# Kernel optimization log

Measured on AMD Instinct MI355X. Metric: run time of the kernel, lower is better.

## Reference

```python
import jax, jax.numpy as jnp
import numpy as np

N = 50000
LN_EPS = 1e-5
NEG_SLOPE = 0.2


def layer_norm(x, w, b):
    mu = jnp.mean(x, axis=-1, keepdims=True)
    var = jnp.mean((x - mu) ** 2, axis=-1, keepdims=True)
    return (x - mu) * jax.lax.rsqrt(var + LN_EPS) * w + b


def gat_conv(x, src, dst, W, a_src, a_dst, bias, concat):
    # W: [in, H*D]; a_src/a_dst: [H, D]
    H, D = a_src.shape
    h = (x @ W).reshape(-1, H, D)                      # [N, H, D]
    s = jnp.einsum('nhd,hd->nh', h, a_src)             # alpha contribution of source
    t = jnp.einsum('nhd,hd->nh', h, a_dst)             # alpha contribution of target
    e = jax.nn.leaky_relu(s[src] + t[dst], NEG_SLOPE)  # [E, H] edge logits
    m = jax.ops.segment_max(e, dst, num_segments=N)    # segment softmax over incoming edges
    p = jnp.exp(e - m[dst])
    z = jax.ops.segment_sum(p, dst, num_segments=N)
    alpha = p / (z[dst] + 1e-16)                       # [E, H]
    out = jax.ops.segment_sum(alpha[:, :, None] * h[src], dst, num_segments=N)  # [N, H, D]
    out = out.reshape(N, H * D) if concat else out.mean(axis=1)
    return out + bias


def setup_inputs() -> dict:
    key = jax.random.key(0)
    ks = jax.random.split(key, 16)
    IN, HID, OUT, H1, H2 = 256, 32, 40, 6, 3
    E = 800000
    g = lambda k, shp, fan: jax.random.normal(k, shp, jnp.float32) * (1.0 / np.sqrt(fan))
    inp = {
        'x': jax.random.normal(ks[0], (N, IN), jnp.float32),
        'edge_index': jax.random.randint(ks[1], (2, E), 0, N, jnp.int32),
        'W1': g(ks[2], (IN, H1 * HID), IN), 'a1s': g(ks[3], (H1, HID), HID), 'a1d': g(ks[4], (H1, HID), HID),
        'b1': jnp.zeros((H1 * HID,), jnp.float32),
        'ln1w': jnp.ones((H1 * HID,), jnp.float32), 'ln1b': jnp.zeros((H1 * HID,), jnp.float32),
        'W2': g(ks[5], (H1 * HID, H2 * HID), H1 * HID), 'a2s': g(ks[6], (H2, HID), HID), 'a2d': g(ks[7], (H2, HID), HID),
        'b2': jnp.zeros((H2 * HID,), jnp.float32),
        'ln2w': jnp.ones((H2 * HID,), jnp.float32), 'ln2b': jnp.zeros((H2 * HID,), jnp.float32),
        'W3': g(ks[8], (H2 * HID, 1 * OUT), H2 * HID), 'a3s': g(ks[9], (1, OUT), OUT), 'a3d': g(ks[10], (1, OUT), OUT),
        'b3': jnp.zeros((OUT,), jnp.float32),
        'ln3w': jnp.ones((OUT,), jnp.float32), 'ln3b': jnp.zeros((OUT,), jnp.float32),
    }
    return inp


def reference(x, edge_index, W1, a1s, a1d, b1, ln1w, ln1b,
              W2, a2s, a2d, b2, ln2w, ln2b,
              W3, a3s, a3d, b3, ln3w, ln3b):
    # add self-loops (PyG GATConv default); eval mode -> dropouts are identity
    loop = jnp.arange(N, dtype=edge_index.dtype)
    src = jnp.concatenate([edge_index[0], loop])
    dst = jnp.concatenate([edge_index[1], loop])

    h = gat_conv(x, src, dst, W1, a1s, a1d, b1, concat=True)
    h = jax.nn.elu(layer_norm(h, ln1w, ln1b))
    h = gat_conv(h, src, dst, W2, a2s, a2d, b2, concat=True)
    h = jax.nn.elu(layer_norm(h, ln2w, ln2b))
    h = gat_conv(h, src, dst, W3, a3s, a3d, b3, concat=False)
    h = layer_norm(h, ln3w, ln3b)
    return jax.nn.log_softmax(h, axis=1)
```

## Files before the change

kernel.cpp:

```cpp
#include <hip/hip_runtime.h>
#include <hip/hip_bf16.h>
#include <cstdint>

#define NNODES 50000
#define NEDGES 800000
#define ETOT   (NEDGES + NNODES)
#define LN_EPS 1e-5f
#define NEG_SLOPE 0.2f
#define ELLW   64

typedef __attribute__((ext_vector_type(8))) short s16x8;
typedef __attribute__((ext_vector_type(4))) float f32x4;

__device__ __forceinline__ float bf2f(unsigned short u) {
    return __uint_as_float(((unsigned int)u) << 16);
}
__device__ __forceinline__ unsigned short f2bf(float f) {
    unsigned int u = __float_as_uint(f);
    u += 0x7FFFu + ((u >> 16) & 1u);
    return (unsigned short)(u >> 16);
}
__device__ __forceinline__ float plo32(unsigned u) { return __uint_as_float(u << 16); }
__device__ __forceinline__ float phi32(unsigned u) { return __uint_as_float(u & 0xffff0000u); }


#define W1SZ (192 * 256)
#define W2SZ (96 * 192)
#define W3SZ (48 * 96)

__global__ __launch_bounds__(256) void prep_kernel(const float* __restrict__ W1, const float* __restrict__ W2,
                                                   const float* __restrict__ W3, unsigned short* __restrict__ wt1,
                                                   unsigned short* __restrict__ wt2, unsigned short* __restrict__ wt3,
                                                   int* __restrict__ counts, int* __restrict__ ell) {
    int i = blockIdx.x * 256 + threadIdx.x;
    if (i < NNODES) {
        counts[i] = 1;
        ell[i * ELLW] = i;
    }
    if (i < W1SZ) {
        int c = i >> 8, k = i & 255;
        int n = c >> 4, r = c & 15;
        wt1[((n * 32 + (k >> 3)) * 16 + r) * 8 + (k & 7)] = f2bf(W1[k * 192 + c]);
    } else if (i < W1SZ + W2SZ) {
        int j = i - W1SZ;
        int c = j / 192, k = j - c * 192;
        int n = c >> 4, r = c & 15;
        wt2[((n * 24 + (k >> 3)) * 16 + r) * 8 + (k & 7)] = f2bf(W2[k * 96 + c]);
    } else if (i < W1SZ + W2SZ + W3SZ) {
        int j = i - (W1SZ + W2SZ);
        int c = j / 96, k = j - c * 96;
        int n = c >> 4, r = c & 15;
        wt3[((n * 12 + (k >> 3)) * 16 + r) * 8 + (k & 7)] = (c < 40) ? f2bf(W3[k * 40 + c]) : (unsigned short)0;
    }
}


__global__ __launch_bounds__(256) void fill_ell_kernel(const int* __restrict__ eidx, int* counts,
                                                       int* __restrict__ ell, int e) {
    int i = blockIdx.x * blockDim.x + threadIdx.x;
    if (i >= e) return;
    int sv = eidx[i];
    int d  = eidx[e + i];
    int slot = atomicAdd(&counts[d], 1);
    if (slot < ELLW) ell[d * ELLW + slot] = sv;
}


template<int K, int F, int CS, int FP, bool ABF>
__global__ __launch_bounds__(256) void mfma_gemm_kernel(const void* __restrict__ Xv,
                                                        const unsigned short* __restrict__ Wt,
                                                        unsigned short* __restrict__ C, int nrows) {
    constexpr int NT = FP / 16;
    int gw = (blockIdx.x * blockDim.x + threadIdx.x) >> 6;
    int lane = threadIdx.x & 63;
    int mbase = gw * 16;
    if (mbase >= nrows) return;
    const int r = lane & 15;
    const int q = lane >> 4;

    f32x4 acc[NT];
#pragma unroll
    for (int n = 0; n < NT; ++n) acc[n] = (f32x4){0.f, 0.f, 0.f, 0.f};

    int arow = mbase + r;
    if (arow >= nrows) arow = nrows - 1;
    const unsigned short* xb = (const unsigned short*)Xv + (size_t)arow * K;
    const float* xf = (const float*)Xv + (size_t)arow * K;

    for (int k0 = 0; k0 < K; k0 += 32) {
        const int kk = k0 + q * 8;
        const unsigned kc = (unsigned)(kk >> 3);
        s16x8 a;
        if constexpr (ABF) {
            a = *reinterpret_cast<const s16x8*>(xb + kk);
        } else {
            float4 lo = *reinterpret_cast<const float4*>(xf + kk);
            float4 hi = *reinterpret_cast<const float4*>(xf + kk + 4);
            a[0] = (short)f2bf(lo.x); a[1] = (short)f2bf(lo.y);
            a[2] = (short)f2bf(lo.z); a[3] = (short)f2bf(lo.w);
            a[4] = (short)f2bf(hi.x); a[5] = (short)f2bf(hi.y);
            a[6] = (short)f2bf(hi.z); a[7] = (short)f2bf(hi.w);
        }
#pragma unroll
        for (int n = 0; n < NT; ++n) {
            s16x8 b = *reinterpret_cast<const s16x8*>(Wt + (((unsigned)n * (K / 8) + kc) * 16 + (unsigned)r) * 8);
            acc[n] = __builtin_amdgcn_mfma_f32_16x16x32_bf16(a, b, acc[n], 0, 0, 0);
        }
    }
#pragma unroll
    for (int n = 0; n < NT; ++n) {
        int col = n * 16 + r;
        if (col < F) {
#pragma unroll
            for (int i = 0; i < 4; ++i) {
                int row = mbase + q * 4 + i;
                if (row < nrows) C[(size_t)row * CS + col] = f2bf(acc[n][i]);
            }
        }
    }
}


template<int H, int D, int FS, int SPAD>
__global__ __launch_bounds__(256) void st_kernel(const unsigned short* __restrict__ feat,
                                                 const float* __restrict__ as, const float* __restrict__ ad,
                                                 float* __restrict__ s, float* __restrict__ tt, int n) {
    int i = blockIdx.x * blockDim.x + threadIdx.x;
    if (i >= n * H) return;
    int h = i % H;
    int node = i / H;
    const ushort4* row = reinterpret_cast<const ushort4*>(feat + (size_t)node * FS + h * D);
    float ss = 0.f, td = 0.f;
#pragma unroll
    for (int d4 = 0; d4 < D / 4; ++d4) {
        ushort4 u = row[d4];
        float v0 = bf2f(u.x), v1 = bf2f(u.y), v2 = bf2f(u.z), v3 = bf2f(u.w);
        int d = d4 * 4;
        ss += v0 * as[h * D + d] + v1 * as[h * D + d + 1] + v2 * as[h * D + d + 2] + v3 * as[h * D + d + 3];
        td += v0 * ad[h * D + d] + v1 * ad[h * D + d + 1] + v2 * ad[h * D + d + 2] + v3 * ad[h * D + d + 3];
    }
    s[node * SPAD + h] = ss;
    tt[i] = td;
}


template<int H, int D, int FS, int CPL, int SPAD, int MODE, typename OutT>
__global__ __launch_bounds__(256) void agg7_kernel(const unsigned short* __restrict__ feat,
                                                   const float* __restrict__ sb, const float* __restrict__ tb,
                                                   const int* __restrict__ counts, const int* __restrict__ ell,
                                                   const float* __restrict__ bias, const float* __restrict__ lnw,
                                                   const float* __restrict__ lnb, OutT* __restrict__ out, int n) {
    constexpr int F = H * D;
    constexpr int NL = F / CPL;
    int wid = (blockIdx.x * blockDim.x + threadIdx.x) >> 6;
    int lane = threadIdx.x & 63;
    if (wid >= n) return;
    const int node = wid;
    const int base = node * ELLW;
    int cnt = counts[node];
    if (cnt > ELLW) cnt = ELLW;
    const bool act = lane < NL;
    const unsigned ch0 = (unsigned)(lane < NL ? lane : 0) * CPL;
    const int h = (int)(ch0 / D);
    const float th = tb[node * H + h];

    float z = 0.f;
    float acc[CPL];
#pragma unroll
    for (int c = 0; c < CPL; ++c) acc[c] = 0.f;

    auto pval = [&](float sv) -> float {
        float e = sv + th;
        e = fmaxf(e, NEG_SLOPE * e);
        return __expf(e);
    };
    auto fmae = [&](float p, const unsigned short* fp) {
        if constexpr (CPL == 4) {
            uint2 w = *reinterpret_cast<const uint2*>(fp);
            acc[0] = fmaf(p, plo32(w.x), acc[0]);
            acc[1] = fmaf(p, phi32(w.x), acc[1]);
            acc[2] = fmaf(p, plo32(w.y), acc[2]);
            acc[3] = fmaf(p, phi32(w.y), acc[3]);
        } else if constexpr (CPL == 2) {
            unsigned w = *reinterpret_cast<const unsigned*>(fp);
            acc[0] = fmaf(p, plo32(w), acc[0]);
            acc[1] = fmaf(p, phi32(w), acc[1]);
        } else {
            acc[0] = fmaf(p, bf2f(*fp), acc[0]);
        }
    };

    int j = 0;
    for (; j + 7 < cnt; j += 8) {
        int4 snA = *reinterpret_cast<const int4*>(ell + base + j);
        int4 snB = *reinterpret_cast<const int4*>(ell + base + j + 4);
        unsigned o0 = (unsigned)snA.x * FS + ch0;
        unsigned o1 = (unsigned)snA.y * FS + ch0;
        unsigned o2 = (unsigned)snA.z * FS + ch0;
        unsigned o3 = (unsigned)snA.w * FS + ch0;
        unsigned o4 = (unsigned)snB.x * FS + ch0;
        unsigned o5 = (unsigned)snB.y * FS + ch0;
        unsigned o6 = (unsigned)snB.z * FS + ch0;
        unsigned o7 = (unsigned)snB.w * FS + ch0;
        if (act) {
            float s0 = sb[(unsigned)snA.x * SPAD + h];
            float s1 = sb[(unsigned)snA.y * SPAD + h];
            float s2 = sb[(unsigned)snA.z * SPAD + h];
            float s3 = sb[(unsigned)snA.w * SPAD + h];
            float s4 = sb[(unsigned)snB.x * SPAD + h];
            float s5 = sb[(unsigned)snB.y * SPAD + h];
            float s6 = sb[(unsigned)snB.z * SPAD + h];
            float s7 = sb[(unsigned)snB.w * SPAD + h];
            if constexpr (CPL == 4) {
                uint2 w0 = *reinterpret_cast<const uint2*>(feat + o0);
                uint2 w1 = *reinterpret_cast<const uint2*>(feat + o1);
                uint2 w2 = *reinterpret_cast<const uint2*>(feat + o2);
                uint2 w3 = *reinterpret_cast<const uint2*>(feat + o3);
                uint2 w4 = *reinterpret_cast<const uint2*>(feat + o4);
                uint2 w5 = *reinterpret_cast<const uint2*>(feat + o5);
                uint2 w6 = *reinterpret_cast<const uint2*>(feat + o6);
                uint2 w7 = *reinterpret_cast<const uint2*>(feat + o7);
                float p0 = pval(s0), p1 = pval(s1), p2 = pval(s2), p3 = pval(s3);
                float p4 = pval(s4), p5 = pval(s5), p6 = pval(s6), p7 = pval(s7);
                z += ((p0 + p1) + (p2 + p3)) + ((p4 + p5) + (p6 + p7));
                acc[0] = fmaf(p0, plo32(w0.x), acc[0]); acc[1] = fmaf(p0, phi32(w0.x), acc[1]);
                acc[2] = fmaf(p0, plo32(w0.y), acc[2]); acc[3] = fmaf(p0, phi32(w0.y), acc[3]);
                acc[0] = fmaf(p1, plo32(w1.x), acc[0]); acc[1] = fmaf(p1, phi32(w1.x), acc[1]);
                acc[2] = fmaf(p1, plo32(w1.y), acc[2]); acc[3] = fmaf(p1, phi32(w1.y), acc[3]);
                acc[0] = fmaf(p2, plo32(w2.x), acc[0]); acc[1] = fmaf(p2, phi32(w2.x), acc[1]);
                acc[2] = fmaf(p2, plo32(w2.y), acc[2]); acc[3] = fmaf(p2, phi32(w2.y), acc[3]);
                acc[0] = fmaf(p3, plo32(w3.x), acc[0]); acc[1] = fmaf(p3, phi32(w3.x), acc[1]);
                acc[2] = fmaf(p3, plo32(w3.y), acc[2]); acc[3] = fmaf(p3, phi32(w3.y), acc[3]);
                acc[0] = fmaf(p4, plo32(w4.x), acc[0]); acc[1] = fmaf(p4, phi32(w4.x), acc[1]);
                acc[2] = fmaf(p4, plo32(w4.y), acc[2]); acc[3] = fmaf(p4, phi32(w4.y), acc[3]);
                acc[0] = fmaf(p5, plo32(w5.x), acc[0]); acc[1] = fmaf(p5, phi32(w5.x), acc[1]);
                acc[2] = fmaf(p5, plo32(w5.y), acc[2]); acc[3] = fmaf(p5, phi32(w5.y), acc[3]);
                acc[0] = fmaf(p6, plo32(w6.x), acc[0]); acc[1] = fmaf(p6, phi32(w6.x), acc[1]);
                acc[2] = fmaf(p6, plo32(w6.y), acc[2]); acc[3] = fmaf(p6, phi32(w6.y), acc[3]);
                acc[0] = fmaf(p7, plo32(w7.x), acc[0]); acc[1] = fmaf(p7, phi32(w7.x), acc[1]);
                acc[2] = fmaf(p7, plo32(w7.y), acc[2]); acc[3] = fmaf(p7, phi32(w7.y), acc[3]);
            } else if constexpr (CPL == 2) {
                unsigned w0 = *reinterpret_cast<const unsigned*>(feat + o0);
                unsigned w1 = *reinterpret_cast<const unsigned*>(feat + o1);
                unsigned w2 = *reinterpret_cast<const unsigned*>(feat + o2);
                unsigned w3 = *reinterpret_cast<const unsigned*>(feat + o3);
                unsigned w4 = *reinterpret_cast<const unsigned*>(feat + o4);
                unsigned w5 = *reinterpret_cast<const unsigned*>(feat + o5);
                unsigned w6 = *reinterpret_cast<const unsigned*>(feat + o6);
                unsigned w7 = *reinterpret_cast<const unsigned*>(feat + o7);
                float p0 = pval(s0), p1 = pval(s1), p2 = pval(s2), p3 = pval(s3);
                float p4 = pval(s4), p5 = pval(s5), p6 = pval(s6), p7 = pval(s7);
                z += ((p0 + p1) + (p2 + p3)) + ((p4 + p5) + (p6 + p7));
                acc[0] = fmaf(p0, plo32(w0), acc[0]); acc[1] = fmaf(p0, phi32(w0), acc[1]);
                acc[0] = fmaf(p1, plo32(w1), acc[0]); acc[1] = fmaf(p1, phi32(w1), acc[1]);
                acc[0] = fmaf(p2, plo32(w2), acc[0]); acc[1] = fmaf(p2, phi32(w2), acc[1]);
                acc[0] = fmaf(p3, plo32(w3), acc[0]); acc[1] = fmaf(p3, phi32(w3), acc[1]);
                acc[0] = fmaf(p4, plo32(w4), acc[0]); acc[1] = fmaf(p4, phi32(w4), acc[1]);
                acc[0] = fmaf(p5, plo32(w5), acc[0]); acc[1] = fmaf(p5, phi32(w5), acc[1]);
                acc[0] = fmaf(p6, plo32(w6), acc[0]); acc[1] = fmaf(p6, phi32(w6), acc[1]);
                acc[0] = fmaf(p7, plo32(w7), acc[0]); acc[1] = fmaf(p7, phi32(w7), acc[1]);
            } else {
                unsigned short w0 = feat[o0], w1 = feat[o1], w2 = feat[o2], w3 = feat[o3];
                unsigned short w4 = feat[o4], w5 = feat[o5], w6 = feat[o6], w7 = feat[o7];
                float p0 = pval(s0), p1 = pval(s1), p2 = pval(s2), p3 = pval(s3);
                float p4 = pval(s4), p5 = pval(s5), p6 = pval(s6), p7 = pval(s7);
                z += ((p0 + p1) + (p2 + p3)) + ((p4 + p5) + (p6 + p7));
                acc[0] = fmaf(p0, bf2f(w0), acc[0]);
                acc[0] = fmaf(p1, bf2f(w1), acc[0]);
                acc[0] = fmaf(p2, bf2f(w2), acc[0]);
                acc[0] = fmaf(p3, bf2f(w3), acc[0]);
                acc[0] = fmaf(p4, bf2f(w4), acc[0]);
                acc[0] = fmaf(p5, bf2f(w5), acc[0]);
                acc[0] = fmaf(p6, bf2f(w6), acc[0]);
                acc[0] = fmaf(p7, bf2f(w7), acc[0]);
            }
        }
    }
    for (; j + 3 < cnt; j += 4) {
        int4 snA = *reinterpret_cast<const int4*>(ell + base + j);
        if (act) {
            float p0 = pval(sb[(unsigned)snA.x * SPAD + h]);
            float p1 = pval(sb[(unsigned)snA.y * SPAD + h]);
            float p2 = pval(sb[(unsigned)snA.z * SPAD + h]);
            float p3 = pval(sb[(unsigned)snA.w * SPAD + h]);
            z += (p0 + p1) + (p2 + p3);
            fmae(p0, feat + (unsigned)snA.x * FS + ch0);
            fmae(p1, feat + (unsigned)snA.y * FS + ch0);
            fmae(p2, feat + (unsigned)snA.z * FS + ch0);
            fmae(p3, feat + (unsigned)snA.w * FS + ch0);
        }
    }
    for (; j < cnt; ++j) {
        int sn = ell[base + j];
        if (act) {
            float p = pval(sb[(unsigned)sn * SPAD + h]);
            z += p;
            fmae(p, feat + (unsigned)sn * FS + ch0);
        }
    }

    const float zinv = 1.f / (z + 1e-16f);
    float v[CPL];
    float sum = 0.f, sumsq = 0.f;
#pragma unroll
    for (int c = 0; c < CPL; ++c) v[c] = 0.f;
    if (act) {
#pragma unroll
        for (int c = 0; c < CPL; ++c) {
            v[c] = fmaf(acc[c], zinv, bias[ch0 + c]);
            sum += v[c];
            sumsq += v[c] * v[c];
        }
    }
#pragma unroll
    for (int off = 32; off; off >>= 1) {
        sum += __shfl_xor(sum, off);
        sumsq += __shfl_xor(sumsq, off);
    }
    const float mu = sum / F;
    const float var = sumsq / F - mu * mu;
    const float rstd = rsqrtf(var + LN_EPS);

    if (MODE == 0) {
        if (act) {
            unsigned short yb[CPL];
#pragma unroll
            for (int c = 0; c < CPL; ++c) {
                float y = (v[c] - mu) * rstd * lnw[ch0 + c] + lnb[ch0 + c];
                y = y > 0.f ? y : expm1f(y);
                yb[c] = f2bf(y);
            }
            OutT* op = out + (size_t)node * F + ch0;
            if constexpr (CPL == 4) {
                ushort4 st = {yb[0], yb[1], yb[2], yb[3]};
                *reinterpret_cast<ushort4*>(op) = st;
            } else if constexpr (CPL == 2) {
                ushort2 st = {yb[0], yb[1]};
                *reinterpret_cast<ushort2*>(op) = st;
            } else {
                *op = yb[0];
            }
        }
    } else {
        float y = 0.f, mx = -1e30f;
        if (act) {
            y = (v[0] - mu) * rstd * lnw[ch0] + lnb[ch0];
            mx = y;
        }
#pragma unroll
        for (int off = 32; off; off >>= 1) mx = fmaxf(mx, __shfl_xor(mx, off));
        float se = act ? __expf(y - mx) : 0.f;
#pragma unroll
        for (int off = 32; off; off >>= 1) se += __shfl_xor(se, off);
        float lse = logf(se);
        if (act) ((float*)out)[(size_t)node * F + ch0] = y - mx - lse;
    }
}


static inline size_t align_up(size_t x) { return (x + 255) & ~(size_t)255; }

extern "C" void kernel_launch(void* const* d_in, const int* in_sizes, int n_in,
                              void* d_out, int out_size, void* d_ws, size_t ws_size,
                              hipStream_t stream) {
    const float* x    = (const float*)d_in[0];
    const int*   eidx = (const int*)d_in[1];
    const float* W1   = (const float*)d_in[2];
    const float* a1s  = (const float*)d_in[3];
    const float* a1d  = (const float*)d_in[4];
    const float* b1   = (const float*)d_in[5];
    const float* ln1w = (const float*)d_in[6];
    const float* ln1b = (const float*)d_in[7];
    const float* W2   = (const float*)d_in[8];
    const float* a2s  = (const float*)d_in[9];
    const float* a2d  = (const float*)d_in[10];
    const float* b2   = (const float*)d_in[11];
    const float* ln2w = (const float*)d_in[12];
    const float* ln2b = (const float*)d_in[13];
    const float* W3   = (const float*)d_in[14];
    const float* a3s  = (const float*)d_in[15];
    const float* a3d  = (const float*)d_in[16];
    const float* b3   = (const float*)d_in[17];
    const float* ln3w = (const float*)d_in[18];
    const float* ln3b = (const float*)d_in[19];

    char* w = (char*)d_ws;
    int* counts = (int*)w;  w += align_up((size_t)NNODES * 4);
    int* ell    = (int*)w;  w += align_up((size_t)NNODES * ELLW * 4);
    unsigned short* bufA = (unsigned short*)w; w += align_up((size_t)NNODES * 192 * 2);
    unsigned short* bufB = (unsigned short*)w; w += align_up((size_t)NNODES * 192 * 2);
    float* sbuf = (float*)w; w += align_up((size_t)NNODES * 8 * 4);
    float* tbuf = (float*)w; w += align_up((size_t)NNODES * 8 * 4);
    unsigned short* wt1 = (unsigned short*)w; w += align_up((size_t)W1SZ * 2);
    unsigned short* wt2 = (unsigned short*)w; w += align_up((size_t)W2SZ * 2);
    unsigned short* wt3 = (unsigned short*)w; w += align_up((size_t)W3SZ * 2);

    const int BS = 256;
    const int PREP_N = W1SZ + W2SZ + W3SZ;
    prep_kernel<<<(PREP_N + BS - 1) / BS, BS, 0, stream>>>(W1, W2, W3, wt1, wt2, wt3, counts, ell);
    fill_ell_kernel<<<(NEDGES + BS - 1) / BS, BS, 0, stream>>>(eidx, counts, ell, NEDGES);

    const int GRID_MM  = ((NNODES + 15) / 16 + 3) / 4;
    const int GRID_AGG = (NNODES + 3) / 4;

    mfma_gemm_kernel<256, 192, 192, 192, false><<<GRID_MM, BS, 0, stream>>>(x, wt1, bufA, NNODES);
    st_kernel<6, 32, 192, 8><<<(NNODES * 6 + BS - 1) / BS, BS, 0, stream>>>(bufA, a1s, a1d, sbuf, tbuf, NNODES);
    agg7_kernel<6, 32, 192, 4, 8, 0, unsigned short><<<GRID_AGG, BS, 0, stream>>>(bufA, sbuf, tbuf, counts, ell, b1, ln1w, ln1b, bufB, NNODES);

    mfma_gemm_kernel<192, 96, 96, 96, true><<<GRID_MM, BS, 0, stream>>>(bufB, wt2, bufA, NNODES);
    st_kernel<3, 32, 96, 4><<<(NNODES * 3 + BS - 1) / BS, BS, 0, stream>>>(bufA, a2s, a2d, sbuf, tbuf, NNODES);
    agg7_kernel<3, 32, 96, 2, 4, 0, unsigned short><<<GRID_AGG, BS, 0, stream>>>(bufA, sbuf, tbuf, counts, ell, b2, ln2w, ln2b, bufB, NNODES);

    mfma_gemm_kernel<96, 40, 64, 48, true><<<GRID_MM, BS, 0, stream>>>(bufB, wt3, bufA, NNODES);
    st_kernel<1, 40, 64, 1><<<(NNODES * 1 + BS - 1) / BS, BS, 0, stream>>>(bufA, a3s, a3d, sbuf, tbuf, NNODES);
    agg7_kernel<1, 40, 64, 1, 1, 1, float><<<GRID_AGG, BS, 0, stream>>>(bufA, sbuf, tbuf, counts, ell, b3, ln3w, ln3b, (float*)d_out, NNODES);
}
```

Baseline: 288.0 us.

## Fuse attention score computation into GEMM epilogue and merge ELL fill into first GEMM

The per-head source/target attention dot products are now computed from the MFMA accumulators in the GEMM epilogue using cross-lane shuffles, which removes the separate st_kernel launches and their re-read of the feature matrix. The ELL adjacency fill is folded into the first GEMM launch as extra blocks, so it runs alongside the GEMM instead of as its own launch. Layer 2's feature row stride also changes from 96 to 128. The trade-offs are more register pressure and shuffle work in the GEMM epilogue, and atomic-heavy fill blocks sharing the GPU with GEMM blocks.

```diff
diff --git a/kernel.cpp b/kernel.cpp
--- a/kernel.cpp
+++ b/kernel.cpp
@@ -55,23 +55,29 @@
 }
 
 
-__global__ __launch_bounds__(256) void fill_ell_kernel(const int* __restrict__ eidx, int* counts,
-                                                       int* __restrict__ ell, int e) {
-    int i = blockIdx.x * blockDim.x + threadIdx.x;
-    if (i >= e) return;
-    int sv = eidx[i];
-    int d  = eidx[e + i];
-    int slot = atomicAdd(&counts[d], 1);
-    if (slot < ELLW) ell[d * ELLW + slot] = sv;
-}
-
-
-template<int K, int F, int CS, int FP, bool ABF>
-__global__ __launch_bounds__(256) void mfma_gemm_kernel(const void* __restrict__ Xv,
-                                                        const unsigned short* __restrict__ Wt,
-                                                        unsigned short* __restrict__ C, int nrows) {
+template<int K, int F, int CS, int FP, int H, int D, int SPAD, bool ABF, bool FILL>
+__global__ __launch_bounds__(256) void gemmst_kernel(const void* __restrict__ Xv,
+                                                     const unsigned short* __restrict__ Wt,
+                                                     unsigned short* __restrict__ C,
+                                                     const float* __restrict__ asf, const float* __restrict__ adf,
+                                                     float* __restrict__ sbuf, float* __restrict__ tbuf,
+                                                     int nrows, int gblocks,
+                                                     const int* __restrict__ eidx, int* counts,
+                                                     int* __restrict__ ell, int e) {
+    if constexpr (FILL) {
+        if (blockIdx.x >= (unsigned)gblocks) {
+            int i = ((int)blockIdx.x - gblocks) * 256 + (int)threadIdx.x;
+            if (i < e) {
+                int sv = eidx[i];
+                int d  = eidx[e + i];
+                int slot = atomicAdd(&counts[d], 1);
+                if (slot < ELLW) ell[d * ELLW + slot] = sv;
+            }
+            return;
+        }
+    }
     constexpr int NT = FP / 16;
-    int gw = (blockIdx.x * blockDim.x + threadIdx.x) >> 6;
+    int gw = (blockIdx.x * 256 + threadIdx.x) >> 6;
     int lane = threadIdx.x & 63;
     int mbase = gw * 16;
     if (mbase >= nrows) return;
@@ -107,6 +113,7 @@
             acc[n] = __builtin_amdgcn_mfma_f32_16x16x32_bf16(a, b, acc[n], 0, 0, 0);
         }
     }
+
 #pragma unroll
     for (int n = 0; n < NT; ++n) {
         int col = n * 16 + r;
@@ -118,29 +125,49 @@
             }
         }
     }
-}
-
-
-template<int H, int D, int FS, int SPAD>
-__global__ __launch_bounds__(256) void st_kernel(const unsigned short* __restrict__ feat,
-                                                 const float* __restrict__ as, const float* __restrict__ ad,
-                                                 float* __restrict__ s, float* __restrict__ tt, int n) {
-    int i = blockIdx.x * blockDim.x + threadIdx.x;
-    if (i >= n * H) return;
-    int h = i % H;
-    int node = i / H;
-    const ushort4* row = reinterpret_cast<const ushort4*>(feat + (size_t)node * FS + h * D);
-    float ss = 0.f, td = 0.f;
-#pragma unroll
-    for (int d4 = 0; d4 < D / 4; ++d4) {
-        ushort4 u = row[d4];
-        float v0 = bf2f(u.x), v1 = bf2f(u.y), v2 = bf2f(u.z), v3 = bf2f(u.w);
-        int d = d4 * 4;
-        ss += v0 * as[h * D + d] + v1 * as[h * D + d + 1] + v2 * as[h * D + d + 2] + v3 * as[h * D + d + 3];
-        td += v0 * ad[h * D + d] + v1 * ad[h * D + d + 1] + v2 * ad[h * D + d + 2] + v3 * ad[h * D + d + 3];
-    }
-    s[node * SPAD + h] = ss;
-    tt[i] = td;
+
+    float ps[4][H], pt[4][H];
+#pragma unroll
+    for (int i = 0; i < 4; ++i)
+#pragma unroll
+        for (int hh = 0; hh < H; ++hh) { ps[i][hh] = 0.f; pt[i][hh] = 0.f; }
+#pragma unroll
+    for (int n = 0; n < NT; ++n) {
+        constexpr int NCOL = 1;
+        (void)NCOL;
+        const int col = n * 16 + r;
+        const int h = (n * 16) / D;
+        float av = (col < F) ? asf[col] : 0.f;
+        float dv = (col < F) ? adf[col] : 0.f;
+#pragma unroll
+        for (int i = 0; i < 4; ++i) {
+            ps[i][h] = fmaf(acc[n][i], av, ps[i][h]);
+            pt[i][h] = fmaf(acc[n][i], dv, pt[i][h]);
+        }
+    }
+#pragma unroll
+    for (int off = 1; off <= 8; off <<= 1) {
+#pragma unroll
+        for (int i = 0; i < 4; ++i)
+#pragma unroll
+            for (int hh = 0; hh < H; ++hh) {
+                ps[i][hh] += __shfl_xor(ps[i][hh], off);
+                pt[i][hh] += __shfl_xor(pt[i][hh], off);
+            }
+    }
+#pragma unroll
+    for (int hh = 0; hh < H; ++hh) {
+        if (r == hh) {
+#pragma unroll
+            for (int i = 0; i < 4; ++i) {
+                int row = mbase + q * 4 + i;
+                if (row < nrows) {
+                    sbuf[row * SPAD + hh] = ps[i][hh];
+                    tbuf[row * H + hh]    = pt[i][hh];
+                }
+            }
+        }
+    }
 }
 
 
@@ -398,20 +425,23 @@
     const int BS = 256;
     const int PREP_N = W1SZ + W2SZ + W3SZ;
     prep_kernel<<<(PREP_N + BS - 1) / BS, BS, 0, stream>>>(W1, W2, W3, wt1, wt2, wt3, counts, ell);
-    fill_ell_kernel<<<(NEDGES + BS - 1) / BS, BS, 0, stream>>>(eidx, counts, ell, NEDGES);
 
     const int GRID_MM  = ((NNODES + 15) / 16 + 3) / 4;
+    const int FILL_NB  = (NEDGES + BS - 1) / BS;
     const int GRID_AGG = (NNODES + 3) / 4;
 
-    mfma_gemm_kernel<256, 192, 192, 192, false><<<GRID_MM, BS, 0, stream>>>(x, wt1, bufA, NNODES);
-    st_kernel<6, 32, 192, 8><<<(NNODES * 6 + BS - 1) / BS, BS, 0, stream>>>(bufA, a1s, a1d, sbuf, tbuf, NNODES);
+    gemmst_kernel<256, 192, 192, 192, 6, 32, 8, false, true>
+        <<<GRID_MM + FILL_NB, BS, 0, stream>>>(x, wt1, bufA, a1s, a1d, sbuf, tbuf, NNODES,
+                                               GRID_MM, eidx, counts, ell, NEDGES);
     agg7_kernel<6, 32, 192, 4, 8, 0, unsigned short><<<GRID_AGG, BS, 0, stream>>>(bufA, sbuf, tbuf, counts, ell, b1, ln1w, ln1b, bufB, NNODES);
 
-    mfma_gemm_kernel<192, 96, 96, 96, true><<<GRID_MM, BS, 0, stream>>>(bufB, wt2, bufA, NNODES);
-    st_kernel<3, 32, 96, 4><<<(NNODES * 3 + BS - 1) / BS, BS, 0, stream>>>(bufA, a2s, a2d, sbuf, tbuf, NNODES);
-    agg7_kernel<3, 32, 96, 2, 4, 0, unsigned short><<<GRID_AGG, BS, 0, stream>>>(bufA, sbuf, tbuf, counts, ell, b2, ln2w, ln2b, bufB, NNODES);
-
-    mfma_gemm_kernel<96, 40, 64, 48, true><<<GRID_MM, BS, 0, stream>>>(bufB, wt3, bufA, NNODES);
-    st_kernel<1, 40, 64, 1><<<(NNODES * 1 + BS - 1) / BS, BS, 0, stream>>>(bufA, a3s, a3d, sbuf, tbuf, NNODES);
+    gemmst_kernel<192, 96, 128, 96, 3, 32, 4, true, false>
+        <<<GRID_MM, BS, 0, stream>>>(bufB, wt2, bufA, a2s, a2d, sbuf, tbuf, NNODES,
+                                     GRID_MM, nullptr, nullptr, nullptr, 0);
+    agg7_kernel<3, 32, 128, 2, 4, 0, unsigned short><<<GRID_AGG, BS, 0, stream>>>(bufA, sbuf, tbuf, counts, ell, b2, ln2w, ln2b, bufB, NNODES);
+
+    gemmst_kernel<96, 40, 64, 48, 1, 40, 1, true, false>
+        <<<GRID_MM, BS, 0, stream>>>(bufB, wt3, bufA, a3s, a3d, sbuf, tbuf, NNODES,
+                                     GRID_MM, nullptr, nullptr, nullptr, 0);
     agg7_kernel<1, 40, 64, 1, 1, 1, float><<<GRID_AGG, BS, 0, stream>>>(bufA, sbuf, tbuf, counts, ell, b3, ln3w, ln3b, (float*)d_out, NNODES);
 }
```

After: 274.9 us. -4.6%, faster.
